# Kernel optimization log

Measured on AMD Instinct MI355X. Metric: run time of the kernel, lower is better.

The kernel has to match this reference:

```python
import jax, jax.numpy as jnp
import numpy as np
import math

N_HEADS = 8


def _grid_sample_bilinear(x, grid):
    """F.grid_sample(x, grid) with bilinear, zero padding, align_corners=False.
    x: [B,C,H,W], grid: [B,Q,N,2] in [-1,1]. Returns [B,Q,N,C] (channels-last)."""
    B, C, H, W = x.shape
    x_nhwc = jnp.transpose(x, (0, 2, 3, 1))  # [B,H,W,C]
    gx = ((grid[..., 0] + 1.0) * W - 1.0) * 0.5  # [B,Q,N]
    gy = ((grid[..., 1] + 1.0) * H - 1.0) * 0.5
    x0 = jnp.floor(gx)
    y0 = jnp.floor(gy)
    fx = gx - x0
    fy = gy - y0
    x0i = x0.astype(jnp.int32)
    y0i = y0.astype(jnp.int32)
    b_idx = jnp.arange(B)[:, None, None]

    def gather(ix, iy):
        valid = (ix >= 0) & (ix < W) & (iy >= 0) & (iy < H)
        v = x_nhwc[b_idx, jnp.clip(iy, 0, H - 1), jnp.clip(ix, 0, W - 1)]  # [B,Q,N,C]
        return v * valid[..., None].astype(x.dtype)

    w00 = ((1.0 - fx) * (1.0 - fy))[..., None]
    w01 = (fx * (1.0 - fy))[..., None]
    w10 = ((1.0 - fx) * fy)[..., None]
    w11 = (fx * fy)[..., None]
    return (gather(x0i, y0i) * w00 + gather(x0i + 1, y0i) * w01 +
            gather(x0i, y0i + 1) * w10 + gather(x0i + 1, y0i + 1) * w11)


def setup_inputs() -> dict:
    key = jax.random.key(0)
    ks = jax.random.split(key, 9)
    B, Q, N, C, H, W = 16, 1000, 16, 256, 100, 100
    x = jax.random.normal(ks[0], (B, C, H, W), dtype=jnp.float32)
    q = jax.random.normal(ks[1], (B, Q, C), dtype=jnp.float32)
    ref_points = jax.random.uniform(ks[2], (B, Q, N, 2), dtype=jnp.float32,
                                    minval=-1.0, maxval=1.0)
    s = 0.02
    wq = jax.random.normal(ks[3], (C, C), dtype=jnp.float32) * s
    bq = jax.random.normal(ks[4], (C,), dtype=jnp.float32) * s
    wk = jax.random.normal(ks[5], (C, C), dtype=jnp.float32) * s
    bk = jax.random.normal(ks[6], (C,), dtype=jnp.float32) * s
    wv = jax.random.normal(ks[7], (C, C), dtype=jnp.float32) * s
    bv = jax.random.normal(ks[8], (C,), dtype=jnp.float32) * s
    return {"x": x, "q": q, "ref_points": ref_points,
            "wq": wq, "bq": bq, "wk": wk, "bk": bk, "wv": wv, "bv": bv}


def reference(x, q, ref_points, wq, bq, wk, bk, wv, bv):
    B, Q, C = q.shape
    N = ref_points.shape[2]
    nh = N_HEADS
    d = C // nh

    qp = q @ wq.T + bq  # [B,Q,C]
    sampled = _grid_sample_bilinear(x, ref_points)          # [B,Q,N,C]
    s = jnp.transpose(sampled, (0, 2, 1, 3))                # [B,N,Q,C] (matches torch transpose(1,-1))
    k = s @ wk.T + bk                                       # [B,N,Q,C]
    v = s @ wv.T + bv

    # Faithful to torch: contiguous [B,N,Q,C] buffer viewed as (B,Q,N,nh,d)
    k = jnp.reshape(k, (B, Q, N, nh, d)).transpose(0, 1, 3, 2, 4)  # [B,Q,nh,N,d]
    v = jnp.reshape(v, (B, Q, N, nh, d)).transpose(0, 1, 3, 2, 4)
    qh = jnp.reshape(qp, (B, Q, nh, d))                            # [B,Q,nh,d]

    attn = jnp.einsum('bqhd,bqhnd->bqhn', qh, k) / math.sqrt(d)
    attn = jax.nn.softmax(attn, axis=-1)
    out = jnp.einsum('bqhn,bqhnd->bqhd', attn, v)
    return out.reshape(B, Q, C)
```

## Files before the change

### kernel.cpp

```cpp
#include <hip/hip_runtime.h>
#include <math.h>

typedef float f4 __attribute__((ext_vector_type(4)));
typedef _Float16 half8 __attribute__((ext_vector_type(8)));

#define C_DIM 256
#define NH 8
#define HD 32
#define Q_DIM 1000
#define N_PTS 16
#define B_DIM 16
#define H_IMG 100
#define W_IMG 100
#define HW 10000
#define BQ2 2
#define NS 32
#define N_QK 2048


__global__ __launch_bounds__(256) void xt_kernel(
    const float* __restrict__ x, _Float16* __restrict__ xt) {
  __shared__ float t[64][65];
  int p0 = blockIdx.x * 64;
  int c0 = blockIdx.y * 64;
  int b = blockIdx.z;
  int tid = threadIdx.x;
  int p4 = tid & 15, cl = tid >> 4;
#pragma unroll
  for (int it = 0; it < 4; ++it) {
    int c = cl + 16 * it;
    int p = p0 + p4 * 4;
    f4 v = {0.f, 0.f, 0.f, 0.f};
    const float* sp = x + ((size_t)b * C_DIM + c0 + c) * HW;
    if (p + 3 < HW) {
      v = *(const f4*)(sp + p);
    } else {
#pragma unroll
      for (int j = 0; j < 4; ++j) if (p + j < HW) v[j] = sp[p + j];
    }
    t[p4 * 4 + 0][c] = v[0];
    t[p4 * 4 + 1][c] = v[1];
    t[p4 * 4 + 2][c] = v[2];
    t[p4 * 4 + 3][c] = v[3];
  }
  __syncthreads();
  int pl = tid >> 2, cq = tid & 3;
  int p = p0 + pl;
  if (p < HW) {
    half8 h0, h1;
#pragma unroll
    for (int j = 0; j < 8; ++j) {
      h0[j] = (_Float16)t[pl][cq * 16 + j];
      h1[j] = (_Float16)t[pl][cq * 16 + 8 + j];
    }
    _Float16* dst = xt + ((size_t)b * HW + p) * C_DIM + c0 + cq * 16;
    *(half8*)dst = h0;
    *(half8*)(dst + 8) = h1;
  }
}

__global__ __launch_bounds__(256) void qconv_kernel(
    const float* __restrict__ q, _Float16* __restrict__ qh) {
  size_t i = ((size_t)blockIdx.x * 256 + threadIdx.x) * 8;
  f4 v0 = *(const f4*)(q + i);
  f4 v1 = *(const f4*)(q + i + 4);
  half8 h;
  h[0] = (_Float16)v0[0]; h[1] = (_Float16)v0[1];
  h[2] = (_Float16)v0[2]; h[3] = (_Float16)v0[3];
  h[4] = (_Float16)v1[0]; h[5] = (_Float16)v1[1];
  h[6] = (_Float16)v1[2]; h[7] = (_Float16)v1[3];
  *(half8*)(qh + i) = h;
}

__global__ __launch_bounds__(256) void prep_wqk(
    const float* __restrict__ wq, const float* __restrict__ wk,
    const float* __restrict__ bq, _Float16* __restrict__ wqkB,
    float* __restrict__ qkb) {
  int n = blockIdx.x;
  int h = n >> 8, cp = n & 255;
  int c = threadIdx.x;
  float acc = 0.f, accb = 0.f;
#pragma unroll 4
  for (int dd = 0; dd < HD; ++dd) {
    float wkv = wk[(size_t)(h * HD + dd) * C_DIM + cp];
    acc += wq[(size_t)(h * HD + dd) * C_DIM + c] * wkv;
    accb += bq[h * HD + dd] * wkv;
  }
  const float s = 0.17677669529663687f;
  wqkB[(size_t)n * C_DIM + c] = (_Float16)(acc * s);
  if (c == 0) qkb[n] = accb * s;
}

__global__ __launch_bounds__(256) void prep_wv(
    const float* __restrict__ wv, _Float16* __restrict__ wvh) {
  int i = blockIdx.x * 256 + threadIdx.x;
  wvh[i] = (_Float16)wv[i];
}

__global__ __launch_bounds__(256) void qk_gemm(
    const _Float16* __restrict__ qh, const _Float16* __restrict__ wqkB,
    const float* __restrict__ qkb, _Float16* __restrict__ qk_g) {
  __shared__ __align__(16) _Float16 lds_buf[2 * 128 * 72];
  _Float16* As = lds_buf;
  _Float16* Bs = lds_buf + 128 * 72;

  int tid = threadIdx.x;
  int m0 = blockIdx.x * 128;
  int n0 = blockIdx.y * 128;
  int wid = tid >> 6, lane = tid & 63;
  int wm = wid >> 1, wn = wid & 1;
  int m_ = lane & 15, kq = lane >> 4;

  f4 acc[4][4];
#pragma unroll
  for (int i = 0; i < 4; ++i)
#pragma unroll
    for (int j = 0; j < 4; ++j) acc[i][j] = {0.f, 0.f, 0.f, 0.f};

#pragma unroll 1
  for (int k0 = 0; k0 < C_DIM; k0 += 64) {
    if (k0) __syncthreads();
#pragma unroll
    for (int j = 0; j < 4; ++j) {
      int idx = j * 256 + tid;
      int r = idx >> 3, kc = idx & 7;
      *(half8*)&As[r * 72 + kc * 8] =
          *(const half8*)(qh + (size_t)(m0 + r) * C_DIM + k0 + kc * 8);
      *(half8*)&Bs[r * 72 + kc * 8] =
          *(const half8*)(wqkB + (size_t)(n0 + r) * C_DIM + k0 + kc * 8);
    }
    __syncthreads();
#pragma unroll
    for (int kk = 0; kk < 64; kk += 32) {
      half8 af[4], bf[4];
#pragma unroll
      for (int mt = 0; mt < 4; ++mt)
        af[mt] = *(const half8*)&As[(wm * 64 + mt * 16 + m_) * 72 + kk + kq * 8];
#pragma unroll
      for (int nt = 0; nt < 4; ++nt)
        bf[nt] = *(const half8*)&Bs[(wn * 64 + nt * 16 + m_) * 72 + kk + kq * 8];
#pragma unroll
      for (int mt = 0; mt < 4; ++mt)
#pragma unroll
        for (int nt = 0; nt < 4; ++nt)
          acc[mt][nt] = __builtin_amdgcn_mfma_f32_16x16x32_f16(
              af[mt], bf[nt], acc[mt][nt], 0, 0, 0);
    }
  }

  __syncthreads();
  _Float16* Cs = lds_buf;
#pragma unroll
  for (int nt = 0; nt < 4; ++nt) {
    int col_l = wn * 64 + nt * 16 + m_;
    float qb = qkb[n0 + col_l];
#pragma unroll
    for (int mt = 0; mt < 4; ++mt) {
      int row_b = wm * 64 + mt * 16 + kq * 4;
#pragma unroll
      for (int r = 0; r < 4; ++r)
        Cs[(row_b + r) * 136 + col_l] = (_Float16)(acc[mt][nt][r] + qb);
    }
  }
  __syncthreads();
#pragma unroll
  for (int j = 0; j < 8; ++j) {
    int idx = j * 256 + tid;
    int r = idx >> 4, cc = idx & 15;
    *(half8*)(qk_g + (size_t)(m0 + r) * N_QK + n0 + cc * 8) =
        *(const half8*)&Cs[r * 136 + cc * 8];
  }
}

__global__ __launch_bounds__(256) void attn_mfma_kernel(
    const _Float16* __restrict__ xt, const float* __restrict__ ref,
    const _Float16* __restrict__ qk_g, _Float16* __restrict__ pv_g) {
  __shared__ __align__(16) _Float16 samp[NS][264];
  __shared__ __align__(16) _Float16 qks[16][264];
  __shared__ float p_s[16][36];

  int tid = threadIdx.x;
  int q2g = blockIdx.x;
  int b = blockIdx.y;
  int q2_0 = q2g * BQ2;
  int m0 = q2g * NS;

  {
    int pair = tid >> 4;
    int col = (tid & 15) * 16;
    int qq = q2_0 + (pair >> 3);
    int hh = pair & 7;
    const _Float16* src = qk_g + ((size_t)b * Q_DIM + qq) * N_QK + hh * C_DIM + col;
    *(half8*)&qks[pair][col] = *(const half8*)src;
    *(half8*)&qks[pair][col + 8] = *(const half8*)(src + 8);
  }

  {
    int s_half = tid >> 5, cl = tid & 31;
    const _Float16* base = xt + (size_t)b * HW * C_DIM + cl * 8;
#pragma unroll 1
    for (int it = 0; it < 4; ++it) {
      int i = it * 8 + s_half;
      int mm = m0 + i;
      int qq = mm % Q_DIM, nn = mm / Q_DIM;
      const float* rp = ref + (((size_t)b * Q_DIM + qq) * N_PTS + nn) * 2;
      float gx = (rp[0] + 1.f) * 50.f - 0.5f;
      float gy = (rp[1] + 1.f) * 50.f - 0.5f;
      float fx0 = floorf(gx), fy0 = floorf(gy);
      float fx = gx - fx0, fy = gy - fy0;
      int ix0 = (int)fx0, iy0 = (int)fy0;
      int ix1 = ix0 + 1, iy1 = iy0 + 1;
      bool x0ok = ix0 >= 0 && ix0 < W_IMG, x1ok = ix1 >= 0 && ix1 < W_IMG;
      bool y0ok = iy0 >= 0 && iy0 < H_IMG, y1ok = iy1 >= 0 && iy1 < H_IMG;
      float acc[8] = {0.f, 0.f, 0.f, 0.f, 0.f, 0.f, 0.f, 0.f};
      if (x0ok && y0ok) {
        half8 v = *(const half8*)(base + (size_t)(iy0 * W_IMG + ix0) * C_DIM);
        float w = (1.f - fx) * (1.f - fy);
#pragma unroll
        for (int j = 0; j < 8; ++j) acc[j] += w * (float)v[j];
      }
      if (x1ok && y0ok) {
        half8 v = *(const half8*)(base + (size_t)(iy0 * W_IMG + ix1) * C_DIM);
        float w = fx * (1.f - fy);
#pragma unroll
        for (int j = 0; j < 8; ++j) acc[j] += w * (float)v[j];
      }
      if (x0ok && y1ok) {
        half8 v = *(const half8*)(base + (size_t)(iy1 * W_IMG + ix0) * C_DIM);
        float w = (1.f - fx) * fy;
#pragma unroll
        for (int j = 0; j < 8; ++j) acc[j] += w * (float)v[j];
      }
      if (x1ok && y1ok) {
        half8 v = *(const half8*)(base + (size_t)(iy1 * W_IMG + ix1) * C_DIM);
        float w = fx * fy;
#pragma unroll
        for (int j = 0; j < 8; ++j) acc[j] += w * (float)v[j];
      }
      half8 o;
#pragma unroll
      for (int j = 0; j < 8; ++j) o[j] = (_Float16)acc[j];
      *(half8*)&samp[i][cl * 8] = o;
    }
  }
  __syncthreads();

  {
    int wid = tid >> 6, lane = tid & 63;
    int m_ = lane & 15, kq = lane >> 4;
    if (wid < 2) {
      f4 d = {0.f, 0.f, 0.f, 0.f};
#pragma unroll
      for (int ks = 0; ks < 8; ++ks) {
        half8 a = *(const half8*)&qks[m_][ks * 32 + kq * 8];
        half8 bfr = *(const half8*)&samp[wid * 16 + m_][ks * 32 + kq * 8];
        d = __builtin_amdgcn_mfma_f32_16x16x32_f16(a, bfr, d, 0, 0, 0);
      }
#pragma unroll
      for (int r = 0; r < 4; ++r) {
        int pair = kq * 4 + r;
        float v = d[r];
        float mx = v;
#pragma unroll
        for (int off = 1; off < 16; off <<= 1) mx = fmaxf(mx, __shfl_xor(mx, off, 16));
        float e = __expf(v - mx);
        float s = e;
#pragma unroll
        for (int off = 1; off < 16; off <<= 1) s += __shfl_xor(s, off, 16);
        if ((pair >> 3) == wid) p_s[pair][wid * 16 + m_] = e / s;
      }
    }
  }
  __syncthreads();

  {
    int chunk = tid & 31, pg = tid >> 5;
    float accA[8] = {0.f, 0.f, 0.f, 0.f, 0.f, 0.f, 0.f, 0.f};
    float accB[8] = {0.f, 0.f, 0.f, 0.f, 0.f, 0.f, 0.f, 0.f};
#pragma unroll 4
    for (int n = 0; n < 16; ++n) {
      half8 s0 = *(const half8*)&samp[n][chunk * 8];
      half8 s1 = *(const half8*)&samp[16 + n][chunk * 8];
      float pA = p_s[pg][n];
      float pB = p_s[pg + 8][16 + n];
#pragma unroll
      for (int j = 0; j < 8; ++j) {
        accA[j] += pA * (float)s0[j];
        accB[j] += pB * (float)s1[j];
      }
    }
    half8 oA, oB;
#pragma unroll
    for (int j = 0; j < 8; ++j) {
      oA[j] = (_Float16)accA[j];
      oB[j] = (_Float16)accB[j];
    }
    _Float16* dst = pv_g + (((size_t)b * Q_DIM + q2_0) * NH + pg) * C_DIM + chunk * 8;
    *(half8*)dst = oA;
    *(half8*)(dst + (size_t)NH * C_DIM) = oB;
  }
}

__global__ __launch_bounds__(256) void proj_kernel(
    const _Float16* __restrict__ pv_g, const _Float16* __restrict__ wvh,
    const float* __restrict__ bv, float* __restrict__ out) {
  int tid = threadIdx.x, lane = tid & 63, wid = tid >> 6;
  int mtile = blockIdx.x;
  int m = lane & 15, kq = lane >> 4;
#pragma unroll 1
  for (int hh = 0; hh < 2; ++hh) {
    int h = wid * 2 + hh;
    half8 af[8];
    const _Float16* arow = pv_g + ((size_t)(mtile * 16 + m) * NH + h) * C_DIM + kq * 8;
#pragma unroll
    for (int ks = 0; ks < 8; ++ks) af[ks] = *(const half8*)(arow + ks * 32);
#pragma unroll 1
    for (int nt = 0; nt < 2; ++nt) {
      int c = h * 32 + nt * 16 + m;
      const _Float16* brow = wvh + (size_t)c * C_DIM + kq * 8;
      f4 acc = {0.f, 0.f, 0.f, 0.f};
#pragma unroll
      for (int ks = 0; ks < 8; ++ks)
        acc = __builtin_amdgcn_mfma_f32_16x16x32_f16(af[ks], *(const half8*)(brow + ks * 32),
                                                     acc, 0, 0, 0);
      float bvv = bv[c];
#pragma unroll
      for (int r = 0; r < 4; ++r)
        out[(size_t)(mtile * 16 + kq * 4 + r) * C_DIM + c] = acc[r] + bvv;
    }
  }
}

__global__ __launch_bounds__(256) void transpose_kernel(
    const float* __restrict__ in, float* __restrict__ out, int rows, int cols) {
  __shared__ float t[32][33];
  size_t off = (size_t)blockIdx.z * rows * cols;
  int r0 = blockIdx.y * 32, c0 = blockIdx.x * 32;
  int tx = threadIdx.x, ty = threadIdx.y;
#pragma unroll
  for (int k = 0; k < 4; ++k) {
    int r = r0 + ty + 8 * k, c = c0 + tx;
    if (r < rows && c < cols) t[ty + 8 * k][tx] = in[off + (size_t)r * cols + c];
  }
  __syncthreads();
#pragma unroll
  for (int k = 0; k < 4; ++k) {
    int c = c0 + ty + 8 * k, r = r0 + tx;
    if (r < rows && c < cols) out[off + (size_t)c * rows + r] = t[tx][ty + 8 * k];
  }
}

__global__ __launch_bounds__(256) void qp_kernel(
    const float* __restrict__ q, const float* __restrict__ wq,
    const float* __restrict__ bq, float* __restrict__ qp) {
  __shared__ float qrows[16][257];
  int row0 = blockIdx.x * 16;
  int tid = threadIdx.x;
  for (int t = tid; t < 16 * C_DIM; t += 256) {
    int r = t >> 8, c = t & 255;
    qrows[r][c] = q[(size_t)(row0 + r) * C_DIM + c];
  }
  __syncthreads();
  float acc[16];
  float b0 = bq[tid];
#pragma unroll
  for (int r = 0; r < 16; ++r) acc[r] = b0;
  const float* wrow = wq + (size_t)tid * C_DIM;
  for (int cc = 0; cc < C_DIM; ++cc) {
    float w = wrow[cc];
#pragma unroll
    for (int r = 0; r < 16; ++r) acc[r] += qrows[r][cc] * w;
  }
#pragma unroll
  for (int r = 0; r < 16; ++r) qp[(size_t)(row0 + r) * C_DIM + tid] = acc[r];
}

__global__ __launch_bounds__(256) void attn_fb_kernel(
    const float* __restrict__ src, int strB, int strY, int strX, int strC,
    const float* __restrict__ ref, const float* __restrict__ qp,
    const float* __restrict__ q, const float* __restrict__ wq,
    const float* __restrict__ bq, const float* __restrict__ wk,
    const float* __restrict__ wv, const float* __restrict__ bv,
    float* __restrict__ out) {
  __shared__ __align__(16) float qp_s[BQ2][C_DIM];
  __shared__ __align__(16) float qk_s[16][260];
  __shared__ __align__(16) float samp_f[NS][260];
  __shared__ float p_f[16][16];
  __shared__ float logit_s[256];

  int tid = threadIdx.x;
  int q2g = blockIdx.x;
  int b = blockIdx.y;
  int q2_0 = q2g * BQ2;
  int m0 = q2g * NS;
  int c4 = tid & 63;
  int grp = tid >> 6;

  if (qp) {
    if (tid < 128) {
      int r = tid >> 6, cc4 = tid & 63;
      *(f4*)&qp_s[r][cc4 * 4] =
          *(const f4*)(qp + ((size_t)b * Q_DIM + q2_0 + r) * C_DIM + cc4 * 4);
    }
  } else {
#pragma unroll
    for (int r = 0; r < BQ2; ++r) {
      float acc = bq[tid];
      const float* qrow = q + ((size_t)b * Q_DIM + q2_0 + r) * C_DIM;
      const float* wrow = wq + (size_t)tid * C_DIM;
      for (int cc = 0; cc < C_DIM; ++cc) acc += qrow[cc] * wrow[cc];
      qp_s[r][tid] = acc;
    }
  }

  {
    int coff = tid * strC;
#pragma unroll 1
    for (int i = 0; i < NS; ++i) {
      int mm = m0 + i;
      int qq = mm % Q_DIM;
      int nn = mm / Q_DIM;
      const float* rp = ref + (((size_t)b * Q_DIM + qq) * N_PTS + nn) * 2;
      float gx = (rp[0] + 1.f) * 50.f - 0.5f;
      float gy = (rp[1] + 1.f) * 50.f - 0.5f;
      float fx0 = floorf(gx), fy0 = floorf(gy);
      float fx = gx - fx0, fy = gy - fy0;
      int ix0 = (int)fx0, iy0 = (int)fy0;
      int ix1 = ix0 + 1, iy1 = iy0 + 1;
      float w00 = (1.f - fx) * (1.f - fy);
      float w01 = fx * (1.f - fy);
      float w10 = (1.f - fx) * fy;
      float w11 = fx * fy;
      size_t bse = (size_t)(b * strB + coff);
      float v = 0.f;
      if (ix0 >= 0 && ix0 < W_IMG) {
        if (iy0 >= 0 && iy0 < H_IMG) v += w00 * src[bse + (size_t)iy0 * strY + (size_t)ix0 * strX];
        if (iy1 >= 0 && iy1 < H_IMG) v += w10 * src[bse + (size_t)iy1 * strY + (size_t)ix0 * strX];
      }
      if (ix1 >= 0 && ix1 < W_IMG) {
        if (iy0 >= 0 && iy0 < H_IMG) v += w01 * src[bse + (size_t)iy0 * strY + (size_t)ix1 * strX];
        if (iy1 >= 0 && iy1 < H_IMG) v += w11 * src[bse + (size_t)iy1 * strY + (size_t)ix1 * strX];
      }
      samp_f[i][tid] = v;
    }
  }
  __syncthreads();

#pragma unroll 1
  for (int hh = 0; hh < 2; ++hh) {
    int h = grp * 2 + hh;
    f4 acc0 = {0.f, 0.f, 0.f, 0.f};
    f4 acc1 = {0.f, 0.f, 0.f, 0.f};
#pragma unroll 2
    for (int dd4 = 0; dd4 < 8; ++dd4) {
      f4 a0 = *(const f4*)&qp_s[0][h * HD + dd4 * 4];
      f4 a1 = *(const f4*)&qp_s[1][h * HD + dd4 * 4];
#pragma unroll
      for (int j = 0; j < 4; ++j) {
        f4 w4 = *(const f4*)(wk + (size_t)(h * HD + dd4 * 4 + j) * C_DIM + c4 * 4);
        acc0 += a0[j] * w4;
        acc1 += a1[j] * w4;
      }
    }
    *(f4*)&qk_s[h][c4 * 4] = acc0;
    *(f4*)&qk_s[8 + h][c4 * 4] = acc1;
  }
  __syncthreads();

  {
    int pair = tid >> 4;
    int n2 = tid & 15;
    int i = (pair >> 3) * 16 + n2;
    float acc = 0.f;
#pragma unroll 4
    for (int cc4 = 0; cc4 < 64; ++cc4) {
      f4 qk4 = *(const f4*)&qk_s[pair][cc4 * 4];
      f4 s4 = *(const f4*)&samp_f[i][cc4 * 4];
      acc += qk4[0] * s4[0] + qk4[1] * s4[1] + qk4[2] * s4[2] + qk4[3] * s4[3];
    }
    logit_s[tid] = acc * 0.17677669529663687f;
  }
  __syncthreads();

  if (tid < 16) {
    float mx = -1e30f;
#pragma unroll
    for (int n2 = 0; n2 < 16; ++n2) mx = fmaxf(mx, logit_s[tid * 16 + n2]);
    float s = 0.f;
    float e[16];
#pragma unroll
    for (int n2 = 0; n2 < 16; ++n2) {
      e[n2] = __expf(logit_s[tid * 16 + n2] - mx);
      s += e[n2];
    }
    float inv = 1.f / s;
#pragma unroll
    for (int n2 = 0; n2 < 16; ++n2) p_f[tid][n2] = e[n2] * inv;
  }
  __syncthreads();

#pragma unroll 1
  for (int k = 0; k < 4; ++k) {
    int pair = k * 4 + grp;
    int roff = (pair >> 3) * 16;
    f4 acc = {0.f, 0.f, 0.f, 0.f};
#pragma unroll
    for (int n2 = 0; n2 < 16; ++n2)
      acc += p_f[pair][n2] * *(const f4*)&samp_f[roff + n2][c4 * 4];
    *(f4*)&qk_s[pair][c4 * 4] = acc;
  }
  __syncthreads();

  {
    int h = tid >> 5;
    float acc0 = 0.f, acc1 = 0.f;
#pragma unroll 4
    for (int cc4 = 0; cc4 < 64; ++cc4) {
      f4 pv0 = *(const f4*)&qk_s[h][cc4 * 4];
      f4 pv1 = *(const f4*)&qk_s[8 + h][cc4 * 4];
      f4 w4 = *(const f4*)(wv + (size_t)tid * C_DIM + cc4 * 4);
      acc0 += pv0[0] * w4[0] + pv0[1] * w4[1] + pv0[2] * w4[2] + pv0[3] * w4[3];
      acc1 += pv1[0] * w4[0] + pv1[1] * w4[1] + pv1[2] * w4[2] + pv1[3] * w4[3];
    }
    float bvv = bv[tid];
    out[((size_t)b * Q_DIM + q2_0) * C_DIM + tid] = acc0 + bvv;
    out[((size_t)b * Q_DIM + q2_0 + 1) * C_DIM + tid] = acc1 + bvv;
  }
}

extern "C" void kernel_launch(void* const* d_in, const int* in_sizes, int n_in,
                              void* d_out, int out_size, void* d_ws, size_t ws_size,
                              hipStream_t stream) {
  const float* x   = (const float*)d_in[0];
  const float* q   = (const float*)d_in[1];
  const float* ref = (const float*)d_in[2];
  const float* wq  = (const float*)d_in[3];
  const float* bq  = (const float*)d_in[4];
  const float* wk  = (const float*)d_in[5];
  const float* wv  = (const float*)d_in[7];
  const float* bv  = (const float*)d_in[8];
  float* out = (float*)d_out;

  const size_t XT_B    = (size_t)B_DIM * HW * C_DIM * 2;
  const size_t QK_B    = (size_t)B_DIM * Q_DIM * N_QK * 2;
  const size_t PV_B    = QK_B;
  const size_t WQKB_B  = (size_t)N_QK * C_DIM * 2;
  const size_t QKB_B   = (size_t)N_QK * 4;
  const size_t WVH_B   = (size_t)C_DIM * C_DIM * 2;
  const size_t NEED    = XT_B + QK_B + PV_B + WQKB_B + QKB_B + WVH_B;

  if (ws_size >= NEED) {
    char* p = (char*)d_ws;
    _Float16* xt    = (_Float16*)p;           p += XT_B;
    _Float16* qk_g  = (_Float16*)p;           p += QK_B;
    _Float16* pv_g  = (_Float16*)p;           p += PV_B;
    _Float16* qh    = (_Float16*)pv_g;
    _Float16* wqkB  = (_Float16*)p;           p += WQKB_B;
    float*    qkb   = (float*)p;              p += QKB_B;
    _Float16* wvh   = (_Float16*)p;

    xt_kernel<<<dim3((HW + 63) / 64, C_DIM / 64, B_DIM), 256, 0, stream>>>(x, xt);
    qconv_kernel<<<(B_DIM * Q_DIM * C_DIM) / (256 * 8), 256, 0, stream>>>(q, qh);
    prep_wqk<<<N_QK, 256, 0, stream>>>(wq, wk, bq, wqkB, qkb);
    prep_wv<<<C_DIM * C_DIM / 256, 256, 0, stream>>>(wv, wvh);
    qk_gemm<<<dim3(B_DIM * Q_DIM / 128, N_QK / 128), 256, 0, stream>>>(qh, wqkB, qkb, qk_g);
    attn_mfma_kernel<<<dim3(Q_DIM / BQ2, B_DIM), 256, 0, stream>>>(xt, ref, qk_g, pv_g);
    proj_kernel<<<B_DIM * Q_DIM / 16, 256, 0, stream>>>(pv_g, wvh, bv, out);
  } else {
    const size_t QP_BYTES = (size_t)B_DIM * Q_DIM * C_DIM * 4;
    const size_t XTF_BYTES = (size_t)B_DIM * HW * C_DIM * 4;
    float* qp = nullptr;
    float* xtf = nullptr;
    if (ws_size >= QP_BYTES) qp = (float*)d_ws;
    if (ws_size >= QP_BYTES + XTF_BYTES) xtf = (float*)((char*)d_ws + QP_BYTES);

    if (xtf) {
      dim3 g((HW + 31) / 32, C_DIM / 32, B_DIM);
      transpose_kernel<<<g, dim3(32, 8), 0, stream>>>(x, xtf, C_DIM, HW);
    }
    if (qp) qp_kernel<<<B_DIM * Q_DIM / 16, 256, 0, stream>>>(q, wq, bq, qp);

    const float* src;
    int sB, sY, sX, sC;
    if (xtf) { src = xtf; sB = HW * C_DIM; sY = W_IMG * C_DIM; sX = C_DIM; sC = 1; }
    else     { src = x;   sB = C_DIM * HW; sY = W_IMG;         sX = 1;     sC = HW; }

    attn_fb_kernel<<<dim3(Q_DIM / BQ2, B_DIM), 256, 0, stream>>>(
        src, sB, sY, sX, sC, ref, qp, q, wq, bq, wk, wv, bv, out);
  }
}
```

Before: 455.5 us.

## Fuse value projection into attention kernel and use packed fp16 accumulation

```diff
diff --git a/kernel.cpp b/kernel.cpp
--- a/kernel.cpp
+++ b/kernel.cpp
@@ -174,7 +174,8 @@
 
 __global__ __launch_bounds__(256) void attn_mfma_kernel(
     const _Float16* __restrict__ xt, const float* __restrict__ ref,
-    const _Float16* __restrict__ qk_g, _Float16* __restrict__ pv_g) {
+    const _Float16* __restrict__ qk_g, const _Float16* __restrict__ wvh,
+    const float* __restrict__ bv, float* __restrict__ out) {
   __shared__ __align__(16) _Float16 samp[NS][264];
   __shared__ __align__(16) _Float16 qks[16][264];
   __shared__ float p_s[16][36];
@@ -184,6 +185,8 @@
   int b = blockIdx.y;
   int q2_0 = q2g * BQ2;
   int m0 = q2g * NS;
+  int wid = tid >> 6, lane = tid & 63;
+  int m_ = lane & 15, kq = lane >> 4;
 
   {
     int pair = tid >> 4;
@@ -212,121 +215,101 @@
       int ix1 = ix0 + 1, iy1 = iy0 + 1;
       bool x0ok = ix0 >= 0 && ix0 < W_IMG, x1ok = ix1 >= 0 && ix1 < W_IMG;
       bool y0ok = iy0 >= 0 && iy0 < H_IMG, y1ok = iy1 >= 0 && iy1 < H_IMG;
-      float acc[8] = {0.f, 0.f, 0.f, 0.f, 0.f, 0.f, 0.f, 0.f};
+      half8 acc = {0, 0, 0, 0, 0, 0, 0, 0};
       if (x0ok && y0ok) {
         half8 v = *(const half8*)(base + (size_t)(iy0 * W_IMG + ix0) * C_DIM);
-        float w = (1.f - fx) * (1.f - fy);
-#pragma unroll
-        for (int j = 0; j < 8; ++j) acc[j] += w * (float)v[j];
+        acc += v * (_Float16)((1.f - fx) * (1.f - fy));
       }
       if (x1ok && y0ok) {
         half8 v = *(const half8*)(base + (size_t)(iy0 * W_IMG + ix1) * C_DIM);
-        float w = fx * (1.f - fy);
-#pragma unroll
-        for (int j = 0; j < 8; ++j) acc[j] += w * (float)v[j];
+        acc += v * (_Float16)(fx * (1.f - fy));
       }
       if (x0ok && y1ok) {
         half8 v = *(const half8*)(base + (size_t)(iy1 * W_IMG + ix0) * C_DIM);
-        float w = (1.f - fx) * fy;
-#pragma unroll
-        for (int j = 0; j < 8; ++j) acc[j] += w * (float)v[j];
+        acc += v * (_Float16)((1.f - fx) * fy);
       }
       if (x1ok && y1ok) {
         half8 v = *(const half8*)(base + (size_t)(iy1 * W_IMG + ix1) * C_DIM);
-        float w = fx * fy;
-#pragma unroll
-        for (int j = 0; j < 8; ++j) acc[j] += w * (float)v[j];
-      }
-      half8 o;
-#pragma unroll
-      for (int j = 0; j < 8; ++j) o[j] = (_Float16)acc[j];
-      *(half8*)&samp[i][cl * 8] = o;
-    }
-  }
-  __syncthreads();
-
-  {
-    int wid = tid >> 6, lane = tid & 63;
-    int m_ = lane & 15, kq = lane >> 4;
-    if (wid < 2) {
-      f4 d = {0.f, 0.f, 0.f, 0.f};
-#pragma unroll
-      for (int ks = 0; ks < 8; ++ks) {
-        half8 a = *(const half8*)&qks[m_][ks * 32 + kq * 8];
-        half8 bfr = *(const half8*)&samp[wid * 16 + m_][ks * 32 + kq * 8];
-        d = __builtin_amdgcn_mfma_f32_16x16x32_f16(a, bfr, d, 0, 0, 0);
-      }
-#pragma unroll
-      for (int r = 0; r < 4; ++r) {
-        int pair = kq * 4 + r;
-        float v = d[r];
-        float mx = v;
-#pragma unroll
-        for (int off = 1; off < 16; off <<= 1) mx = fmaxf(mx, __shfl_xor(mx, off, 16));
-        float e = __expf(v - mx);
-        float s = e;
-#pragma unroll
-        for (int off = 1; off < 16; off <<= 1) s += __shfl_xor(s, off, 16);
-        if ((pair >> 3) == wid) p_s[pair][wid * 16 + m_] = e / s;
-      }
+        acc += v * (_Float16)(fx * fy);
+      }
+      *(half8*)&samp[i][cl * 8] = acc;
+    }
+  }
+  __syncthreads();
+
+  if (wid < 2) {
+    f4 d = {0.f, 0.f, 0.f, 0.f};
+#pragma unroll
+    for (int ks = 0; ks < 8; ++ks) {
+      half8 a = *(const half8*)&qks[m_][ks * 32 + kq * 8];
+      half8 bfr = *(const half8*)&samp[wid * 16 + m_][ks * 32 + kq * 8];
+      d = __builtin_amdgcn_mfma_f32_16x16x32_f16(a, bfr, d, 0, 0, 0);
+    }
+#pragma unroll
+    for (int r = 0; r < 4; ++r) {
+      int pair = kq * 4 + r;
+      float v = d[r];
+      float mx = v;
+#pragma unroll
+      for (int off = 1; off < 16; off <<= 1) mx = fmaxf(mx, __shfl_xor(mx, off, 16));
+      float e = __expf(v - mx);
+      float s = e;
+#pragma unroll
+      for (int off = 1; off < 16; off <<= 1) s += __shfl_xor(s, off, 16);
+      if ((pair >> 3) == wid) p_s[pair][wid * 16 + m_] = e / s;
     }
   }
   __syncthreads();
 
   {
     int chunk = tid & 31, pg = tid >> 5;
-    float accA[8] = {0.f, 0.f, 0.f, 0.f, 0.f, 0.f, 0.f, 0.f};
-    float accB[8] = {0.f, 0.f, 0.f, 0.f, 0.f, 0.f, 0.f, 0.f};
-#pragma unroll 4
-    for (int n = 0; n < 16; ++n) {
-      half8 s0 = *(const half8*)&samp[n][chunk * 8];
-      half8 s1 = *(const half8*)&samp[16 + n][chunk * 8];
-      float pA = p_s[pg][n];
-      float pB = p_s[pg + 8][16 + n];
-#pragma unroll
-      for (int j = 0; j < 8; ++j) {
-        accA[j] += pA * (float)s0[j];
-        accB[j] += pB * (float)s1[j];
-      }
-    }
-    half8 oA, oB;
-#pragma unroll
-    for (int j = 0; j < 8; ++j) {
-      oA[j] = (_Float16)accA[j];
-      oB[j] = (_Float16)accB[j];
-    }
-    _Float16* dst = pv_g + (((size_t)b * Q_DIM + q2_0) * NH + pg) * C_DIM + chunk * 8;
-    *(half8*)dst = oA;
-    *(half8*)(dst + (size_t)NH * C_DIM) = oB;
-  }
-}
-
-__global__ __launch_bounds__(256) void proj_kernel(
-    const _Float16* __restrict__ pv_g, const _Float16* __restrict__ wvh,
-    const float* __restrict__ bv, float* __restrict__ out) {
-  int tid = threadIdx.x, lane = tid & 63, wid = tid >> 6;
-  int mtile = blockIdx.x;
-  int m = lane & 15, kq = lane >> 4;
-#pragma unroll 1
-  for (int hh = 0; hh < 2; ++hh) {
-    int h = wid * 2 + hh;
+    half8 aA0 = {0,0,0,0,0,0,0,0}, aA1 = aA0, aB0 = aA0, aB1 = aA0;
+#pragma unroll
+    for (int n = 0; n < 16; n += 2) {
+      half8 s0a = *(const half8*)&samp[n][chunk * 8];
+      half8 s0b = *(const half8*)&samp[n + 1][chunk * 8];
+      half8 s1a = *(const half8*)&samp[16 + n][chunk * 8];
+      half8 s1b = *(const half8*)&samp[17 + n][chunk * 8];
+      aA0 += s0a * (_Float16)p_s[pg][n];
+      aA1 += s0b * (_Float16)p_s[pg][n + 1];
+      aB0 += s1a * (_Float16)p_s[pg + 8][16 + n];
+      aB1 += s1b * (_Float16)p_s[pg + 8][17 + n];
+    }
+    half8 oA = aA0 + aA1;
+    half8 oB = aB0 + aB1;
+    __syncthreads();
+    *(half8*)&qks[pg][chunk * 8] = oA;
+    *(half8*)&qks[8 + pg][chunk * 8] = oB;
+  }
+  __syncthreads();
+
+  {
     half8 af[8];
-    const _Float16* arow = pv_g + ((size_t)(mtile * 16 + m) * NH + h) * C_DIM + kq * 8;
-#pragma unroll
-    for (int ks = 0; ks < 8; ++ks) af[ks] = *(const half8*)(arow + ks * 32);
-#pragma unroll 1
-    for (int nt = 0; nt < 2; ++nt) {
-      int c = h * 32 + nt * 16 + m;
-      const _Float16* brow = wvh + (size_t)c * C_DIM + kq * 8;
-      f4 acc = {0.f, 0.f, 0.f, 0.f};
-#pragma unroll
-      for (int ks = 0; ks < 8; ++ks)
-        acc = __builtin_amdgcn_mfma_f32_16x16x32_f16(af[ks], *(const half8*)(brow + ks * 32),
-                                                     acc, 0, 0, 0);
-      float bvv = bv[c];
-#pragma unroll
-      for (int r = 0; r < 4; ++r)
-        out[(size_t)(mtile * 16 + kq * 4 + r) * C_DIM + c] = acc[r] + bvv;
+#pragma unroll
+    for (int ks = 0; ks < 8; ++ks)
+      af[ks] = *(const half8*)&qks[m_][ks * 32 + kq * 8];
+#pragma unroll
+    for (int hh = 0; hh < 2; ++hh) {
+      int h = wid * 2 + hh;
+#pragma unroll
+      for (int nt = 0; nt < 2; ++nt) {
+        int c = h * 32 + nt * 16 + m_;
+        const _Float16* brow = wvh + (size_t)c * C_DIM + kq * 8;
+        f4 acc = {0.f, 0.f, 0.f, 0.f};
+#pragma unroll
+        for (int ks = 0; ks < 8; ++ks)
+          acc = __builtin_amdgcn_mfma_f32_16x16x32_f16(
+              af[ks], *(const half8*)(brow + ks * 32), acc, 0, 0, 0);
+        float bvv = bv[c];
+#pragma unroll
+        for (int r = 0; r < 4; ++r) {
+          int row = kq * 4 + r;
+          if (row == h)
+            out[((size_t)b * Q_DIM + q2_0) * C_DIM + c] = acc[r] + bvv;
+          if (row == h + 8)
+            out[((size_t)b * Q_DIM + q2_0 + 1) * C_DIM + c] = acc[r] + bvv;
+        }
+      }
     }
   }
 }
@@ -543,18 +526,17 @@
 
   const size_t XT_B    = (size_t)B_DIM * HW * C_DIM * 2;
   const size_t QK_B    = (size_t)B_DIM * Q_DIM * N_QK * 2;
-  const size_t PV_B    = QK_B;
+  const size_t QH_B    = (size_t)B_DIM * Q_DIM * C_DIM * 2;
   const size_t WQKB_B  = (size_t)N_QK * C_DIM * 2;
   const size_t QKB_B   = (size_t)N_QK * 4;
   const size_t WVH_B   = (size_t)C_DIM * C_DIM * 2;
-  const size_t NEED    = XT_B + QK_B + PV_B + WQKB_B + QKB_B + WVH_B;
+  const size_t NEED    = XT_B + QK_B + QH_B + WQKB_B + QKB_B + WVH_B;
 
   if (ws_size >= NEED) {
     char* p = (char*)d_ws;
     _Float16* xt    = (_Float16*)p;           p += XT_B;
     _Float16* qk_g  = (_Float16*)p;           p += QK_B;
-    _Float16* pv_g  = (_Float16*)p;           p += PV_B;
-    _Float16* qh    = (_Float16*)pv_g;
+    _Float16* qh    = (_Float16*)p;           p += QH_B;
     _Float16* wqkB  = (_Float16*)p;           p += WQKB_B;
     float*    qkb   = (float*)p;              p += QKB_B;
     _Float16* wvh   = (_Float16*)p;
@@ -564,8 +546,8 @@
     prep_wqk<<<N_QK, 256, 0, stream>>>(wq, wk, bq, wqkB, qkb);
     prep_wv<<<C_DIM * C_DIM / 256, 256, 0, stream>>>(wv, wvh);
     qk_gemm<<<dim3(B_DIM * Q_DIM / 128, N_QK / 128), 256, 0, stream>>>(qh, wqkB, qkb, qk_g);
-    attn_mfma_kernel<<<dim3(Q_DIM / BQ2, B_DIM), 256, 0, stream>>>(xt, ref, qk_g, pv_g);
-    proj_kernel<<<B_DIM * Q_DIM / 16, 256, 0, stream>>>(pv_g, wvh, bv, out);
+    attn_mfma_kernel<<<dim3(Q_DIM / BQ2, B_DIM), 256, 0, stream>>>(
+        xt, ref, qk_g, wvh, bv, out);
   } else {
     const size_t QP_BYTES = (size_t)B_DIM * Q_DIM * C_DIM * 4;
     const size_t XTF_BYTES = (size_t)B_DIM * HW * C_DIM * 4;
```

After: 517.4 us. +13.6%, slower.
